# Kernel tuning notes

Hardware: AMD Instinct MI355X
Metric: run time of the kernel (lower is better)

## Reference

```python
import jax, jax.numpy as jnp
import numpy as np

B = 512      # batch (len(missing_type))
HALF = 12    # prompt_length // 3
D = 12       # prompt_depth
DT = 512     # text embed dim
DI = 768     # image embed dim
E = DT + DI  # 1280, concat dim
R = 16
H = E // R    # 80
HC = DT // R  # 32
EPS = 1e-5


def _ln(x, g, b):
    m = jnp.mean(x, -1, keepdims=True)
    v = jnp.mean((x - m) ** 2, -1, keepdims=True)
    return (x - m) * jax.lax.rsqrt(v + EPS) * g + b


def _mlp(x, w1, b1, w2, b2):
    return jax.nn.gelu(x @ w1 + b1, approximate=False) @ w2 + b2


def setup_inputs() -> dict:
    key = jax.random.key(0)
    ks = jax.random.split(key, 20)
    n = lambda k, s: jax.random.normal(k, s, dtype=jnp.float32) * 0.02
    return {
        "missing_type": jax.random.randint(ks[0], (B,), 0, 3),
        "vpc": n(ks[1], (HALF, DI)), "vpm": n(ks[2], (HALF, DI)),
        "tpc": n(ks[3], (HALF, DT)), "tpm": n(ks[4], (HALF, DT)),
        "cpc": n(ks[5], (HALF, DT)), "cpi": n(ks[6], (HALF, DT)), "cpt": n(ks[7], (HALF, DT)),
        "ln_img_g": jnp.ones((D, E)), "ln_img_b": jnp.zeros((D, E)),
        "ln_txt_g": jnp.ones((D, E)), "ln_txt_b": jnp.zeros((D, E)),
        "img_w1": n(ks[8], (D, E, H)), "img_b1": jnp.zeros((D, H)),
        "img_w2": n(ks[9], (D, H, DI)), "img_b2": jnp.zeros((D, DI)),
        "txt_w1": n(ks[10], (D, E, H)), "txt_b1": jnp.zeros((D, H)),
        "txt_w2": n(ks[11], (D, H, DT)), "txt_b2": jnp.zeros((D, DT)),
        "cimg_w1": n(ks[12], (DT, HC)), "cimg_b1": jnp.zeros((HC,)),
        "cimg_w2": n(ks[13], (HC, DI)), "cimg_b2": jnp.zeros((DI,)),
        "ctxt_w1": n(ks[14], (DT, HC)), "ctxt_b1": jnp.zeros((HC,)),
        "ctxt_w2": n(ks[15], (HC, DT)), "ctxt_b2": jnp.zeros((DT,)),
    }


def reference(missing_type, vpc, vpm, tpc, tpm, cpc, cpi, cpt,
              ln_img_g, ln_img_b, ln_txt_g, ln_txt_b,
              img_w1, img_b1, img_w2, img_b2,
              txt_w1, txt_b1, txt_w2, txt_b2,
              cimg_w1, cimg_b1, cimg_w2, cimg_b2,
              ctxt_w1, ctxt_b1, ctxt_w2, ctxt_b2):
    depth = img_w1.shape[0]
    mt = missing_type
    # per-sample branch selection, vectorized over the batch
    img = jnp.where((mt == 2)[:, None, None], vpm[None], vpc[None])  # [B,HALF,768]
    txt = jnp.where((mt == 1)[:, None, None], tpm[None], tpc[None])  # [B,HALF,512]
    common = jnp.stack([cpc, cpi, cpt])[mt]                          # [B,HALF,512]
    imgs, txts = [], []
    for d in range(depth):  # sequential depth dependency
        x = jnp.concatenate([img, txt], -1)  # [B,HALF,1280]
        img = _mlp(_ln(x, ln_img_g[d], ln_img_b[d]), img_w1[d], img_b1[d], img_w2[d], img_b2[d])
        txt = _mlp(_ln(x, ln_txt_g[d], ln_txt_b[d]), txt_w1[d], txt_b1[d], txt_w2[d], txt_b2[d])
        imgs.append(img)
        txts.append(txt)
    # depth-0 prompts get the projected common prompt appended along tokens
    img0 = jnp.concatenate([imgs[0], _mlp(common, cimg_w1, cimg_b1, cimg_w2, cimg_b2)], axis=1)
    txt0 = jnp.concatenate([txts[0], _mlp(common, ctxt_w1, ctxt_b1, ctxt_w2, ctxt_b2)], axis=1)
    return (img0, txt0, jnp.stack(imgs[1:]), jnp.stack(txts[1:]))
```

## Files before the change

### kernel.cpp

```cpp
#include <hip/hip_runtime.h>

typedef unsigned int u32;
typedef unsigned short u16;

#define TPB 640

namespace {
constexpr size_t F_WP1  = 0;
constexpr size_t F_WP2  = 1228800;
constexpr size_t F_S1   = 1843200;
constexpr size_t F_T1   = 1845120;
constexpr size_t F_XI_P = 1847040;
constexpr size_t F_XT_P = 2178816;
constexpr size_t F_CI_P = 2400000;
constexpr size_t F_CT_P = 2427648;
constexpr size_t F_END_P = 2446080;
constexpr size_t F_XI_U = 0;
constexpr size_t F_XT_U = 331776;
constexpr size_t F_CI_U = 552960;
constexpr size_t F_CT_U = 580608;
}

__device__ __forceinline__ float bflo(u32 u) { return __uint_as_float(u << 16); }
__device__ __forceinline__ float bfhi(u32 u) { return __uint_as_float(u & 0xffff0000u); }
__device__ __forceinline__ float gelu_f(float x) { return 0.5f * x * (1.0f + erff(x * 0.70710678118654752f)); }
__device__ __forceinline__ u16 f2bf(float f) {
    u32 u = __float_as_uint(f);
    u += 0x7fffu + ((u >> 16) & 1u);
    return (u16)(u >> 16);
}

struct P {
    const float *vpc, *vpm, *tpc, *tpm, *cpc, *cpi, *cpt;
    const float *lig, *lib, *ltg, *ltb;
    const float *iw1, *ib1, *iw2, *ib2;
    const float *tw1, *tb1, *tw2, *tb2;
    const float *ciw1, *cib1, *ciw2, *cib2;
    const float *ctw1, *ctb1, *ctw2, *ctb2;
    const u16 *wp1, *wp2;
    const float *s1, *t1;
    float *xi, *xt, *cimg, *ctxt;
};

__global__ __launch_bounds__(320) void prep_kernel(P p, u16* wp1o, u32* wp2o, float* s1o, float* t1o) {
    __shared__ float sA[4][80], sB[4][80];
    const int t = threadIdx.x;
    if (blockIdx.x < 24) {
        const int d = blockIdx.x >> 1, path = blockIdx.x & 1;
        const float* W1 = (path ? p.tw1 : p.iw1) + (size_t)d * 1280 * 80;
        const float* G  = (path ? p.ltg : p.lig) + d * 1280;
        const float* Bb = (path ? p.ltb : p.lib) + d * 1280;
        const int j = t % 80, kc = t / 80;
        float S = 0.f, T = 0.f;
        for (int k = kc * 320; k < kc * 320 + 320; ++k) {
            float w = W1[(size_t)k * 80 + j];
            float wg = G[k] * w;
            S += wg; T += Bb[k] * w;
            wp1o[((size_t)(d * 1280) + k) * 160 + path * 80 + j] = f2bf(wg);
        }
        sA[kc][j] = S; sB[kc][j] = T;
        __syncthreads();
        if (t < 80) {
            float Ssum = sA[0][t] + sA[1][t] + sA[2][t] + sA[3][t];
            float Tsum = sB[0][t] + sB[1][t] + sB[2][t] + sB[3][t];
            s1o[d * 160 + path * 80 + t] = Ssum;
            t1o[d * 160 + path * 80 + t] = Tsum + (path ? p.tb1 : p.ib1)[d * 80 + t];
        }
    } else {
        constexpr u32 N2 = 12u * 80 * 640;
        u32 i = (blockIdx.x - 24) * 320 + t;
        if (i >= N2) return;
        u32 c2 = i % 640, rem = i / 640;
        u32 k = rem % 80, d = rem / 80;
        u32 c0 = 2 * c2;
        const float* s = (c0 < 768) ? (p.iw2 + ((size_t)(d * 80) + k) * 768 + c0)
                                    : (p.tw2 + ((size_t)(d * 80) + k) * 512 + (c0 - 768));
        float2 v = *reinterpret_cast<const float2*>(s);
        wp2o[i] = (u32)f2bf(v.x) | ((u32)f2bf(v.y) << 16);
    }
}

__global__ __launch_bounds__(TPB) void chain2_kernel(P p) {
    __shared__ float smem[6608];
    float* sx   = smem;
    float* part = smem + 1280;
    float* hh   = smem + 6400;
    float* redA = smem + 6560;
    float* redB = smem + 6580;
    float* st   = smem + 6600;

    const int tid = threadIdx.x;
    const int blk = blockIdx.x;

    if (blk < 36) {
        const int v = blk / 12, t = blk % 12;
        const float* is = (v == 2) ? p.vpm : p.vpc;
        const float* ts = (v == 1) ? p.tpm : p.tpc;
        for (int k = tid; k < 768; k += TPB) sx[k] = is[t * 768 + k];
        if (tid < 512) sx[768 + tid] = ts[t * 512 + tid];
        __syncthreads();

        for (int d = 0; d < 12; ++d) {
            {
                float x0 = sx[tid], x1 = sx[tid + 640];
                float s = x0 + x1, s2 = x0 * x0 + x1 * x1;
                #pragma unroll
                for (int off = 32; off > 0; off >>= 1) { s += __shfl_down(s, off); s2 += __shfl_down(s2, off); }
                if ((tid & 63) == 0) { redA[tid >> 6] = s; redB[tid >> 6] = s2; }
            }
            __syncthreads();
            if (tid == 0) {
                float S = 0.f, S2 = 0.f;
                #pragma unroll
                for (int w = 0; w < 10; ++w) { S += redA[w]; S2 += redB[w]; }
                float m = S * (1.0f / 1280.0f);
                float var = S2 * (1.0f / 1280.0f) - m * m;
                st[0] = m; st[1] = rsqrtf(var + 1e-5f);
            }
            {
                const int g = tid % 20, kc = tid / 20;
                const int j0 = 8 * g, k0 = 40 * kc;
                const u16* wp = p.wp1 + ((size_t)(d * 1280) + k0) * 160 + j0;
                float a0 = 0.f, a1 = 0.f, a2 = 0.f, a3 = 0.f;
                float a4 = 0.f, a5 = 0.f, a6 = 0.f, a7 = 0.f;
                #pragma unroll 8
                for (int i = 0; i < 40; ++i) {
                    uint4 w = *reinterpret_cast<const uint4*>(wp);
                    float xv = sx[k0 + i];
                    a0 += xv * bflo(w.x); a1 += xv * bfhi(w.x);
                    a2 += xv * bflo(w.y); a3 += xv * bfhi(w.y);
                    a4 += xv * bflo(w.z); a5 += xv * bfhi(w.z);
                    a6 += xv * bflo(w.w); a7 += xv * bfhi(w.w);
                    wp += 160;
                }
                *reinterpret_cast<float4*>(part + kc * 160 + j0)     = make_float4(a0, a1, a2, a3);
                *reinterpret_cast<float4*>(part + kc * 160 + j0 + 4) = make_float4(a4, a5, a6, a7);
            }
            __syncthreads();
            if (tid < 160) {
                float y = 0.f;
                #pragma unroll
                for (int kc = 0; kc < 32; ++kc) y += part[kc * 160 + tid];
                const float m = st[0], rs = st[1];
                float hpre = rs * y - m * rs * p.s1[d * 160 + tid] + p.t1[d * 160 + tid];
                hh[tid] = gelu_f(hpre);
            }
            __syncthreads();
            {
                const int g2 = tid % 320, kc = tid / 320;
                const int c0 = 4 * g2, k0 = 40 * kc;
                const u16* wq = p.wp2 + ((size_t)(d * 80) + k0) * 1280 + c0;
                const float* hb = hh + ((c0 >= 768) ? 80 : 0);
                float a0 = 0.f, a1 = 0.f, a2 = 0.f, a3 = 0.f;
                #pragma unroll 8
                for (int i = 0; i < 40; ++i) {
                    uint2 w = *reinterpret_cast<const uint2*>(wq);
                    float hv = hb[k0 + i];
                    a0 += hv * bflo(w.x); a1 += hv * bfhi(w.x);
                    a2 += hv * bflo(w.y); a3 += hv * bfhi(w.y);
                    wq += 1280;
                }
                *reinterpret_cast<float4*>(part + kc * 1280 + c0) = make_float4(a0, a1, a2, a3);
            }
            __syncthreads();
            {
                const int c0 = 2 * tid;
                const int pth = (c0 >= 768);
                const int cc = c0 - 768 * pth;
                const int Np = pth ? 512 : 768;
                float2 bb = *reinterpret_cast<const float2*>((pth ? p.tb2 : p.ib2) + d * Np + cc);
                float a0 = part[c0]     + part[1280 + c0]     + bb.x;
                float a1 = part[c0 + 1] + part[1280 + c0 + 1] + bb.y;
                __syncthreads();
                sx[c0] = a0; sx[c0 + 1] = a1;
                float* xo = pth ? (p.xt + ((size_t)(d * 36) + blk) * 512 + cc)
                                : (p.xi + ((size_t)(d * 36) + blk) * 768 + cc);
                *reinterpret_cast<float2*>(xo) = make_float2(a0, a1);
            }
            __syncthreads();
        }
    } else {
        float* cx  = smem;
        float* ph  = smem + 512;
        float* hhl = smem + 768;
        const int rr = blk - 36, v = rr / 12, t = rr % 12;
        const float* cs = (v == 0) ? p.cpc : (v == 1) ? p.cpi : p.cpt;
        if (tid < 512) cx[tid] = cs[t * 512 + tid];
        __syncthreads();
        if (tid < 256) {
            const int o = tid & 63, kc = tid >> 6;
            const int path = o >> 5, j = o & 31;
            const float* w = (path ? p.ctw1 : p.ciw1) + (size_t)(kc * 128) * 32 + j;
            float a = 0.f;
            #pragma unroll 8
            for (int i = 0; i < 128; ++i) { a += cx[kc * 128 + i] * (*w); w += 32; }
            ph[kc * 64 + o] = a;
        }
        __syncthreads();
        if (tid < 64) {
            const int path = tid >> 5, j = tid & 31;
            float a = (path ? p.ctb1 : p.cib1)[j];
            #pragma unroll
            for (int kc = 0; kc < 4; ++kc) a += ph[kc * 64 + tid];
            hhl[tid] = gelu_f(a);
        }
        __syncthreads();
        for (int o = tid; o < 1280; o += TPB) {
            if (o < 768) {
                float a = p.cib2[o];
                #pragma unroll
                for (int k = 0; k < 32; ++k) a += hhl[k] * p.ciw2[k * 768 + o];
                p.cimg[rr * 768 + o] = a;
            } else {
                const int oo = o - 768;
                float a = p.ctb2[oo];
                #pragma unroll
                for (int k = 0; k < 32; ++k) a += hhl[32 + k] * p.ctw2[k * 512 + oo];
                p.ctxt[rr * 512 + oo] = a;
            }
        }
    }
}

__global__ __launch_bounds__(TPB) void chain_fb_kernel(P p) {
    __shared__ float smem[6592];
    float* sx   = smem;
    float* xln0 = smem + 1280;
    float* xln1 = smem + 2560;
    float* part = smem + 3840;
    float* hh   = smem + 6400;
    float* redA = smem + 6560;
    float* redB = smem + 6570;
    float* st   = smem + 6580;

    const int tid = threadIdx.x;
    const int blk = blockIdx.x;

    if (blk < 36) {
        const int v = blk / 12, t = blk % 12;
        const float* is = (v == 2) ? p.vpm : p.vpc;
        const float* ts = (v == 1) ? p.tpm : p.tpc;
        if (tid < 512) sx[768 + tid] = ts[t * 512 + tid];
        for (int k = tid; k < 768; k += TPB) sx[k] = is[t * 768 + k];
        __syncthreads();
        for (int d = 0; d < 12; ++d) {
            {
                float x0 = sx[tid], x1 = sx[tid + 640];
                float s = x0 + x1, s2 = x0 * x0 + x1 * x1;
                #pragma unroll
                for (int off = 32; off > 0; off >>= 1) { s += __shfl_down(s, off); s2 += __shfl_down(s2, off); }
                if ((tid & 63) == 0) { redA[tid >> 6] = s; redB[tid >> 6] = s2; }
            }
            __syncthreads();
            if (tid == 0) {
                float S = 0.f, S2 = 0.f;
                #pragma unroll
                for (int w = 0; w < 10; ++w) { S += redA[w]; S2 += redB[w]; }
                float m = S * (1.0f / 1280.0f);
                float var = S2 * (1.0f / 1280.0f) - m * m;
                st[0] = m; st[1] = rsqrtf(var + 1e-5f);
            }
            __syncthreads();
            const float m = st[0], rs = st[1];
            #pragma unroll
            for (int q = 0; q < 2; ++q) {
                const int k = tid + 640 * q;
                float xc = (sx[k] - m) * rs;
                xln0[k] = xc * p.lig[d * 1280 + k] + p.lib[d * 1280 + k];
                xln1[k] = xc * p.ltg[d * 1280 + k] + p.ltb[d * 1280 + k];
            }
            __syncthreads();
            {
                const int g = tid % 40, kc = tid / 40;
                const int j0 = 4 * g;
                const float* xl = (j0 >= 80) ? xln1 : xln0;
                const int k0 = kc * 80;
                float a0 = 0.f, a1 = 0.f, a2 = 0.f, a3 = 0.f;
                const float* wp = (j0 < 80) ? (p.iw1 + ((size_t)(d * 1280) + k0) * 80 + j0)
                                            : (p.tw1 + ((size_t)(d * 1280) + k0) * 80 + (j0 - 80));
                #pragma unroll 8
                for (int i = 0; i < 80; ++i) {
                    float4 w = *reinterpret_cast<const float4*>(wp);
                    float xv = xl[k0 + i];
                    a0 += xv * w.x; a1 += xv * w.y; a2 += xv * w.z; a3 += xv * w.w;
                    wp += 80;
                }
                *reinterpret_cast<float4*>(part + kc * 160 + j0) = make_float4(a0, a1, a2, a3);
            }
            __syncthreads();
            if (tid < 160) {
                const int path = tid >= 80, j = tid - 80 * path;
                float a = (path ? p.tb1 : p.ib1)[d * 80 + j];
                #pragma unroll
                for (int kc = 0; kc < 16; ++kc) a += part[kc * 160 + tid];
                hh[tid] = gelu_f(a);
            }
            __syncthreads();
            {
                const int c = tid;
                const int pth = (c >= 384);
                const int cc = 2 * c - 768 * pth;
                const float* hb = hh + 80 * pth;
                const int Np = pth ? 512 : 768;
                const float* b2 = (pth ? p.tb2 : p.ib2) + d * Np + cc;
                float a0 = b2[0], a1 = b2[1];
                const float* wp = (pth ? p.tw2 + (size_t)(d * 80) * 512 : p.iw2 + (size_t)(d * 80) * 768) + cc;
                #pragma unroll 16
                for (int k = 0; k < 80; ++k) {
                    float2 w = *reinterpret_cast<const float2*>(wp);
                    float hv = hb[k];
                    a0 += hv * w.x; a1 += hv * w.y;
                    wp += Np;
                }
                sx[2 * c] = a0; sx[2 * c + 1] = a1;
                float* xo = pth ? (p.xt + ((size_t)(d * 36) + blk) * 512 + cc)
                                : (p.xi + ((size_t)(d * 36) + blk) * 768 + cc);
                *reinterpret_cast<float2*>(xo) = make_float2(a0, a1);
            }
            __syncthreads();
        }
    } else {
        float* cx  = smem;
        float* ph  = smem + 512;
        float* hhl = smem + 768;
        const int rr = blk - 36, v = rr / 12, t = rr % 12;
        const float* cs = (v == 0) ? p.cpc : (v == 1) ? p.cpi : p.cpt;
        if (tid < 512) cx[tid] = cs[t * 512 + tid];
        __syncthreads();
        if (tid < 256) {
            const int o = tid & 63, kc = tid >> 6;
            const int path = o >> 5, j = o & 31;
            const float* w = (path ? p.ctw1 : p.ciw1) + (size_t)(kc * 128) * 32 + j;
            float a = 0.f;
            #pragma unroll 8
            for (int i = 0; i < 128; ++i) { a += cx[kc * 128 + i] * (*w); w += 32; }
            ph[kc * 64 + o] = a;
        }
        __syncthreads();
        if (tid < 64) {
            const int path = tid >> 5, j = tid & 31;
            float a = (path ? p.ctb1 : p.cib1)[j];
            #pragma unroll
            for (int kc = 0; kc < 4; ++kc) a += ph[kc * 64 + tid];
            hhl[tid] = gelu_f(a);
        }
        __syncthreads();
        for (int o = tid; o < 1280; o += TPB) {
            if (o < 768) {
                float a = p.cib2[o];
                #pragma unroll
                for (int k = 0; k < 32; ++k) a += hhl[k] * p.ciw2[k * 768 + o];
                p.cimg[rr * 768 + o] = a;
            } else {
                const int oo = o - 768;
                float a = p.ctb2[oo];
                #pragma unroll
                for (int k = 0; k < 32; ++k) a += hhl[32 + k] * p.ctw2[k * 512 + oo];
                p.ctxt[rr * 512 + oo] = a;
            }
        }
    }
}

__global__ __launch_bounds__(256) void emit_kernel(const int* __restrict__ mt,
                                                   const float* __restrict__ xi,
                                                   const float* __restrict__ xt,
                                                   const float* __restrict__ cimg,
                                                   const float* __restrict__ ctxt,
                                                   float* __restrict__ out) {
    constexpr unsigned int C0 = 512u * 24 * 192;
    constexpr unsigned int C1 = 512u * 24 * 128;
    constexpr unsigned int C2 = 11u * 512 * 12 * 192;
    constexpr unsigned int C3 = 11u * 512 * 12 * 128;
    constexpr unsigned int TOT = C0 + C1 + C2 + C3;
    const unsigned int stride = gridDim.x * blockDim.x;
    for (unsigned int c = blockIdx.x * blockDim.x + threadIdx.x; c < TOT; c += stride) {
        const float* src;
        if (c < C0) {
            unsigned int b = c / 4608u, r = c % 4608u;
            unsigned int tok = r / 192u, col = (r % 192u) * 4u;
            int v = mt[b];
            src = (tok < 12u) ? xi + ((size_t)v * 12 + tok) * 768 + col
                              : cimg + ((size_t)v * 12 + (tok - 12u)) * 768 + col;
        } else if (c < C0 + C1) {
            unsigned int cc = c - C0;
            unsigned int b = cc / 3072u, r = cc % 3072u;
            unsigned int tok = r / 128u, col = (r % 128u) * 4u;
            int v = mt[b];
            src = (tok < 12u) ? xt + ((size_t)v * 12 + tok) * 512 + col
                              : ctxt + ((size_t)v * 12 + (tok - 12u)) * 512 + col;
        } else if (c < C0 + C1 + C2) {
            unsigned int cc = c - C0 - C1;
            unsigned int d = cc / 1179648u, r = cc % 1179648u;
            unsigned int b = r / 2304u, rr = r % 2304u;
            unsigned int tok = rr / 192u, col = (rr % 192u) * 4u;
            int v = mt[b];
            src = xi + ((size_t)(d + 1) * 36 + v * 12 + tok) * 768 + col;
        } else {
            unsigned int cc = c - C0 - C1 - C2;
            unsigned int d = cc / 786432u, r = cc % 786432u;
            unsigned int b = r / 1536u, rr = r % 1536u;
            unsigned int tok = rr / 128u, col = (rr % 128u) * 4u;
            int v = mt[b];
            src = xt + ((size_t)(d + 1) * 36 + v * 12 + tok) * 512 + col;
        }
        *reinterpret_cast<float4*>(out + (size_t)c * 4) = *reinterpret_cast<const float4*>(src);
    }
}

extern "C" void kernel_launch(void* const* d_in, const int* in_sizes, int n_in,
                              void* d_out, int out_size, void* d_ws, size_t ws_size,
                              hipStream_t stream) {
    const int* mt = (const int*)d_in[0];
    float* ws = (float*)d_ws;
    P p;
    p.vpc  = (const float*)d_in[1];
    p.vpm  = (const float*)d_in[2];
    p.tpc  = (const float*)d_in[3];
    p.tpm  = (const float*)d_in[4];
    p.cpc  = (const float*)d_in[5];
    p.cpi  = (const float*)d_in[6];
    p.cpt  = (const float*)d_in[7];
    p.lig  = (const float*)d_in[8];
    p.lib  = (const float*)d_in[9];
    p.ltg  = (const float*)d_in[10];
    p.ltb  = (const float*)d_in[11];
    p.iw1  = (const float*)d_in[12];
    p.ib1  = (const float*)d_in[13];
    p.iw2  = (const float*)d_in[14];
    p.ib2  = (const float*)d_in[15];
    p.tw1  = (const float*)d_in[16];
    p.tb1  = (const float*)d_in[17];
    p.tw2  = (const float*)d_in[18];
    p.tb2  = (const float*)d_in[19];
    p.ciw1 = (const float*)d_in[20];
    p.cib1 = (const float*)d_in[21];
    p.ciw2 = (const float*)d_in[22];
    p.cib2 = (const float*)d_in[23];
    p.ctw1 = (const float*)d_in[24];
    p.ctb1 = (const float*)d_in[25];
    p.ctw2 = (const float*)d_in[26];
    p.ctb2 = (const float*)d_in[27];

    const bool packed = (ws_size >= F_END_P * sizeof(float));
    if (packed) {
        p.wp1  = (const u16*)(ws + F_WP1);
        p.wp2  = (const u16*)(ws + F_WP2);
        p.s1   = ws + F_S1;
        p.t1   = ws + F_T1;
        p.xi   = ws + F_XI_P;
        p.xt   = ws + F_XT_P;
        p.cimg = ws + F_CI_P;
        p.ctxt = ws + F_CT_P;
        constexpr u32 N2 = 12u * 80 * 640;
        const int nb = 24 + (N2 + 319) / 320;
        prep_kernel<<<dim3(nb), dim3(320), 0, stream>>>(p, (u16*)(ws + F_WP1), (u32*)(ws + F_WP2),
                                                        ws + F_S1, ws + F_T1);
        chain2_kernel<<<dim3(72), dim3(TPB), 0, stream>>>(p);
    } else {
        p.wp1 = nullptr; p.wp2 = nullptr; p.s1 = nullptr; p.t1 = nullptr;
        p.xi   = ws + F_XI_U;
        p.xt   = ws + F_XT_U;
        p.cimg = ws + F_CI_U;
        p.ctxt = ws + F_CT_U;
        chain_fb_kernel<<<dim3(72), dim3(TPB), 0, stream>>>(p);
    }
    emit_kernel<<<dim3(4096), dim3(256), 0, stream>>>(mt, p.xi, p.xt, p.cimg, p.ctxt, (float*)d_out);
}
```

Before: 268.4 us.

## Stream per-depth bf16 weight slots into LDS with double-buffered async loads

Repacks both MLP weight matrices into one contiguous per-depth blob of fifteen 40KB slots. The chain kernel prefetches the next slot into LDS with global_load_lds while computing on the current one, replacing direct strided global weight reads. The prep work is split into a fully parallel pack kernel and a separate LN-fold reduction kernel, and the second GEMV no longer needs a cross-thread partial sum. This adds a barrier and vmcnt wait per slot, about 92KB of dynamic LDS per block, and an extra kernel launch.

```diff
diff --git a/kernel.cpp b/kernel.cpp
--- a/kernel.cpp
+++ b/kernel.cpp
@@ -4,21 +4,20 @@
 typedef unsigned short u16;
 
 #define TPB 640
+#define NSLOT_TOT 180
+#define SLOT_F32 10240
+#define CHAIN_DYN 92928
 
 namespace {
-constexpr size_t F_WP1  = 0;
-constexpr size_t F_WP2  = 1228800;
+constexpr size_t F_BLOB = 0;
 constexpr size_t F_S1   = 1843200;
 constexpr size_t F_T1   = 1845120;
-constexpr size_t F_XI_P = 1847040;
-constexpr size_t F_XT_P = 2178816;
-constexpr size_t F_CI_P = 2400000;
-constexpr size_t F_CT_P = 2427648;
-constexpr size_t F_END_P = 2446080;
-constexpr size_t F_XI_U = 0;
-constexpr size_t F_XT_U = 331776;
-constexpr size_t F_CI_U = 552960;
-constexpr size_t F_CT_U = 580608;
+constexpr size_t F_XI   = 1847040;
+constexpr size_t F_XT   = 2178816;
+constexpr size_t F_CI   = 2400000;
+constexpr size_t F_CT   = 2427648;
+constexpr size_t F_END  = 2446080;
+constexpr size_t F_XI_U = 0, F_XT_U = 331776, F_CI_U = 552960, F_CT_U = 580608;
 }
 
 __device__ __forceinline__ float bflo(u32 u) { return __uint_as_float(u << 16); }
@@ -37,68 +36,104 @@
     const float *tw1, *tb1, *tw2, *tb2;
     const float *ciw1, *cib1, *ciw2, *cib2;
     const float *ctw1, *ctb1, *ctw2, *ctb2;
-    const u16 *wp1, *wp2;
+    const u16 *blob;
     const float *s1, *t1;
     float *xi, *xt, *cimg, *ctxt;
 };
 
-__global__ __launch_bounds__(320) void prep_kernel(P p, u16* wp1o, u32* wp2o, float* s1o, float* t1o) {
-    __shared__ float sA[4][80], sB[4][80];
-    const int t = threadIdx.x;
-    if (blockIdx.x < 24) {
-        const int d = blockIdx.x >> 1, path = blockIdx.x & 1;
-        const float* W1 = (path ? p.tw1 : p.iw1) + (size_t)d * 1280 * 80;
-        const float* G  = (path ? p.ltg : p.lig) + d * 1280;
-        const float* Bb = (path ? p.ltb : p.lib) + d * 1280;
-        const int j = t % 80, kc = t / 80;
-        float S = 0.f, T = 0.f;
-        for (int k = kc * 320; k < kc * 320 + 320; ++k) {
-            float w = W1[(size_t)k * 80 + j];
-            float wg = G[k] * w;
-            S += wg; T += Bb[k] * w;
-            wp1o[((size_t)(d * 1280) + k) * 160 + path * 80 + j] = f2bf(wg);
-        }
-        sA[kc][j] = S; sB[kc][j] = T;
-        __syncthreads();
-        if (t < 80) {
-            float Ssum = sA[0][t] + sA[1][t] + sA[2][t] + sA[3][t];
-            float Tsum = sB[0][t] + sB[1][t] + sB[2][t] + sB[3][t];
-            s1o[d * 160 + path * 80 + t] = Ssum;
-            t1o[d * 160 + path * 80 + t] = Tsum + (path ? p.tb1 : p.ib1)[d * 80 + t];
-        }
+__global__ __launch_bounds__(256) void prep_pack_kernel(P p, u32* blob32) {
+    constexpr u32 N1 = 12u * 1280 * 80;
+    constexpr u32 N2 = 12u * 80 * 640;
+    u32 i = blockIdx.x * 256 + threadIdx.x;
+    if (i < N1) {
+        u32 j2 = i % 80, rem = i / 80;
+        u32 k = rem % 1280, d = rem / 1280;
+        u32 j0 = 2 * j2;
+        const int path = (j0 >= 80);
+        const float* W = (path ? p.tw1 : p.iw1) + ((size_t)(d * 1280) + k) * 80 + (j0 - 80 * path);
+        float g = (path ? p.ltg : p.lig)[d * 1280 + k];
+        float2 v = *reinterpret_cast<const float2*>(W);
+        blob32[(size_t)d * 153600 + (size_t)k * 80 + j2] =
+            (u32)f2bf(g * v.x) | ((u32)f2bf(g * v.y) << 16);
     } else {
-        constexpr u32 N2 = 12u * 80 * 640;
-        u32 i = (blockIdx.x - 24) * 320 + t;
-        if (i >= N2) return;
-        u32 c2 = i % 640, rem = i / 640;
+        u32 ii = i - N1;
+        if (ii >= N2) return;
+        u32 c2 = ii % 640, rem = ii / 640;
         u32 k = rem % 80, d = rem / 80;
         u32 c0 = 2 * c2;
         const float* s = (c0 < 768) ? (p.iw2 + ((size_t)(d * 80) + k) * 768 + c0)
                                     : (p.tw2 + ((size_t)(d * 80) + k) * 512 + (c0 - 768));
         float2 v = *reinterpret_cast<const float2*>(s);
-        wp2o[i] = (u32)f2bf(v.x) | ((u32)f2bf(v.y) << 16);
-    }
-}
-
-__global__ __launch_bounds__(TPB) void chain2_kernel(P p) {
-    __shared__ float smem[6608];
-    float* sx   = smem;
-    float* part = smem + 1280;
-    float* hh   = smem + 6400;
-    float* redA = smem + 6560;
-    float* redB = smem + 6580;
-    float* st   = smem + 6600;
-
+        blob32[(size_t)d * 153600 + 102400 + (size_t)k * 640 + c2] =
+            (u32)f2bf(v.x) | ((u32)f2bf(v.y) << 16);
+    }
+}
+
+__global__ __launch_bounds__(TPB) void prep_fold_kernel(P p, float* s1o, float* t1o) {
+    __shared__ float sA[8][80], sB[8][80];
     const int tid = threadIdx.x;
-    const int blk = blockIdx.x;
+    const int d = blockIdx.x >> 1, path = blockIdx.x & 1;
+    const float* W1 = (path ? p.tw1 : p.iw1) + (size_t)d * 1280 * 80;
+    const float* G  = (path ? p.ltg : p.lig) + d * 1280;
+    const float* Bb = (path ? p.ltb : p.lib) + d * 1280;
+    const int j = tid % 80, kc = tid / 80;
+    float S = 0.f, T = 0.f;
+    for (int k = kc * 160; k < kc * 160 + 160; ++k) {
+        float w = W1[(size_t)k * 80 + j];
+        S += G[k] * w; T += Bb[k] * w;
+    }
+    sA[kc][j] = S; sB[kc][j] = T;
+    __syncthreads();
+    if (tid < 80) {
+        float Ss = 0.f, Ts = 0.f;
+        #pragma unroll
+        for (int q = 0; q < 8; ++q) { Ss += sA[q][tid]; Ts += sB[q][tid]; }
+        s1o[d * 160 + path * 80 + tid] = Ss;
+        t1o[d * 160 + path * 80 + tid] = Ts + (path ? p.tb1 : p.ib1)[d * 80 + tid];
+    }
+}
+
+__device__ __forceinline__ void stage_slot(const u16* blob, float* buf, int sigma) {
+    const int d = sigma / 15, s = sigma % 15;
+    const char* gbase = (const char*)(blob + (size_t)d * 307200
+                                      + (s < 10 ? (size_t)s * 20480 : 204800 + (size_t)(s - 10) * 20480));
+    char* lbase = (char*)buf;
+    const int lane = threadIdx.x & 63, wave = threadIdx.x >> 6;
+    #pragma unroll
+    for (int r = 0; r < 4; ++r) {
+        const int q = r * 10 + wave;
+        __builtin_amdgcn_global_load_lds(
+            (const __attribute__((address_space(1))) void*)(gbase + q * 1024 + lane * 16),
+            (__attribute__((address_space(3))) void*)(lbase + q * 1024), 16, 0, 0);
+    }
+}
+
+#define SLOT_SYNC do { asm volatile("s_waitcnt vmcnt(0)" ::: "memory"); \
+                       __builtin_amdgcn_sched_barrier(0); __syncthreads(); } while (0)
+
+__global__ __launch_bounds__(TPB) void chain4_kernel(P p) {
+    extern __shared__ float smem[];
+    float* buf0 = smem;
+    float* buf1 = smem + 10240;
+    float* sx   = smem + 20480;
+    float* part = smem + 21760;
+    float* hh   = smem + 23040;
+    float* redA = smem + 23200;
+    float* redB = smem + 23210;
+    float* st   = smem + 23220;
+
+    const int tid = threadIdx.x, blk = blockIdx.x;
 
     if (blk < 36) {
         const int v = blk / 12, t = blk % 12;
+        stage_slot(p.blob, buf0, 0);
         const float* is = (v == 2) ? p.vpm : p.vpc;
         const float* ts = (v == 1) ? p.tpm : p.tpc;
         for (int k = tid; k < 768; k += TPB) sx[k] = is[t * 768 + k];
         if (tid < 512) sx[768 + tid] = ts[t * 512 + tid];
-        __syncthreads();
+        SLOT_SYNC;
+        int cur = 0;
+        const int jp = tid % 80, kc = tid / 80;
 
         for (int d = 0; d < 12; ++d) {
             {
@@ -117,65 +152,53 @@
                 float var = S2 * (1.0f / 1280.0f) - m * m;
                 st[0] = m; st[1] = rsqrtf(var + 1e-5f);
             }
-            {
-                const int g = tid % 20, kc = tid / 20;
-                const int j0 = 8 * g, k0 = 40 * kc;
-                const u16* wp = p.wp1 + ((size_t)(d * 1280) + k0) * 160 + j0;
-                float a0 = 0.f, a1 = 0.f, a2 = 0.f, a3 = 0.f;
-                float a4 = 0.f, a5 = 0.f, a6 = 0.f, a7 = 0.f;
-                #pragma unroll 8
-                for (int i = 0; i < 40; ++i) {
-                    uint4 w = *reinterpret_cast<const uint4*>(wp);
-                    float xv = sx[k0 + i];
-                    a0 += xv * bflo(w.x); a1 += xv * bfhi(w.x);
-                    a2 += xv * bflo(w.y); a3 += xv * bfhi(w.y);
-                    a4 += xv * bflo(w.z); a5 += xv * bfhi(w.z);
-                    a6 += xv * bflo(w.w); a7 += xv * bfhi(w.w);
-                    wp += 160;
+            float a0 = 0.f, a1 = 0.f, b0 = 0.f, b1 = 0.f;
+            for (int s = 0; s < 10; ++s) {
+                const int sig = d * 15 + s;
+                if (sig + 1 < NSLOT_TOT) stage_slot(p.blob, cur ? buf0 : buf1, sig + 1);
+                const u32* wp = (const u32*)(cur ? buf1 : buf0) + kc * 1280 + jp;
+                const float* xs = sx + s * 128 + kc * 16;
+                #pragma unroll
+                for (int i = 0; i < 16; ++i) {
+                    u32 w = wp[i * 80];
+                    float xv = xs[i];
+                    a0 += xv * bflo(w); a1 += xv * bfhi(w);
                 }
-                *reinterpret_cast<float4*>(part + kc * 160 + j0)     = make_float4(a0, a1, a2, a3);
-                *reinterpret_cast<float4*>(part + kc * 160 + j0 + 4) = make_float4(a4, a5, a6, a7);
-            }
-            __syncthreads();
+                if (s == 9) { part[kc * 160 + 2 * jp] = a0; part[kc * 160 + 2 * jp + 1] = a1; }
+                SLOT_SYNC; cur ^= 1;
+            }
             if (tid < 160) {
                 float y = 0.f;
                 #pragma unroll
-                for (int kc = 0; kc < 32; ++kc) y += part[kc * 160 + tid];
+                for (int q = 0; q < 8; ++q) y += part[q * 160 + tid];
                 const float m = st[0], rs = st[1];
-                float hpre = rs * y - m * rs * p.s1[d * 160 + tid] + p.t1[d * 160 + tid];
-                hh[tid] = gelu_f(hpre);
-            }
-            __syncthreads();
-            {
-                const int g2 = tid % 320, kc = tid / 320;
-                const int c0 = 4 * g2, k0 = 40 * kc;
-                const u16* wq = p.wp2 + ((size_t)(d * 80) + k0) * 1280 + c0;
-                const float* hb = hh + ((c0 >= 768) ? 80 : 0);
-                float a0 = 0.f, a1 = 0.f, a2 = 0.f, a3 = 0.f;
-                #pragma unroll 8
-                for (int i = 0; i < 40; ++i) {
-                    uint2 w = *reinterpret_cast<const uint2*>(wq);
-                    float hv = hb[k0 + i];
-                    a0 += hv * bflo(w.x); a1 += hv * bfhi(w.x);
-                    a2 += hv * bflo(w.y); a3 += hv * bfhi(w.y);
-                    wq += 1280;
+                hh[tid] = gelu_f(rs * y - m * rs * p.s1[d * 160 + tid] + p.t1[d * 160 + tid]);
+            }
+            __syncthreads();
+            for (int s = 10; s < 15; ++s) {
+                const int sig = d * 15 + s;
+                if (sig + 1 < NSLOT_TOT) stage_slot(p.blob, cur ? buf0 : buf1, sig + 1);
+                const u32* wq = (const u32*)(cur ? buf1 : buf0) + tid;
+                const float* hb = hh + ((tid >= 384) ? 80 : 0) + (s - 10) * 16;
+                #pragma unroll
+                for (int i = 0; i < 16; ++i) {
+                    u32 w = wq[i * 640];
+                    float hv = hb[i];
+                    b0 += hv * bflo(w); b1 += hv * bfhi(w);
                 }
-                *reinterpret_cast<float4*>(part + kc * 1280 + c0) = make_float4(a0, a1, a2, a3);
-            }
-            __syncthreads();
+                SLOT_SYNC; cur ^= 1;
+            }
             {
                 const int c0 = 2 * tid;
                 const int pth = (c0 >= 768);
                 const int cc = c0 - 768 * pth;
                 const int Np = pth ? 512 : 768;
-                float2 bb = *reinterpret_cast<const float2*>((pth ? p.tb2 : p.ib2) + d * Np + cc);
-                float a0 = part[c0]     + part[1280 + c0]     + bb.x;
-                float a1 = part[c0 + 1] + part[1280 + c0 + 1] + bb.y;
-                __syncthreads();
-                sx[c0] = a0; sx[c0 + 1] = a1;
+                const float* bb = (pth ? p.tb2 : p.ib2) + d * Np + cc;
+                float o0 = b0 + bb[0], o1 = b1 + bb[1];
+                sx[c0] = o0; sx[c0 + 1] = o1;
                 float* xo = pth ? (p.xt + ((size_t)(d * 36) + blk) * 512 + cc)
                                 : (p.xi + ((size_t)(d * 36) + blk) * 768 + cc);
-                *reinterpret_cast<float2*>(xo) = make_float2(a0, a1);
+                *reinterpret_cast<float2*>(xo) = make_float2(o0, o1);
             }
             __syncthreads();
         }
@@ -188,20 +211,20 @@
         if (tid < 512) cx[tid] = cs[t * 512 + tid];
         __syncthreads();
         if (tid < 256) {
-            const int o = tid & 63, kc = tid >> 6;
+            const int o = tid & 63, kcq = tid >> 6;
             const int path = o >> 5, j = o & 31;
-            const float* w = (path ? p.ctw1 : p.ciw1) + (size_t)(kc * 128) * 32 + j;
+            const float* w = (path ? p.ctw1 : p.ciw1) + (size_t)(kcq * 128) * 32 + j;
             float a = 0.f;
             #pragma unroll 8
-            for (int i = 0; i < 128; ++i) { a += cx[kc * 128 + i] * (*w); w += 32; }
-            ph[kc * 64 + o] = a;
+            for (int i = 0; i < 128; ++i) { a += cx[kcq * 128 + i] * (*w); w += 32; }
+            ph[kcq * 64 + o] = a;
         }
         __syncthreads();
         if (tid < 64) {
             const int path = tid >> 5, j = tid & 31;
             float a = (path ? p.ctb1 : p.cib1)[j];
             #pragma unroll
-            for (int kc = 0; kc < 4; ++kc) a += ph[kc * 64 + tid];
+            for (int q = 0; q < 4; ++q) a += ph[q * 64 + tid];
             hhl[tid] = gelu_f(a);
         }
         __syncthreads();
@@ -232,10 +255,7 @@
     float* redA = smem + 6560;
     float* redB = smem + 6570;
     float* st   = smem + 6580;
-
-    const int tid = threadIdx.x;
-    const int blk = blockIdx.x;
-
+    const int tid = threadIdx.x, blk = blockIdx.x;
     if (blk < 36) {
         const int v = blk / 12, t = blk % 12;
         const float* is = (v == 2) ? p.vpm : p.vpc;
@@ -271,10 +291,10 @@
             }
             __syncthreads();
             {
-                const int g = tid % 40, kc = tid / 40;
+                const int g = tid % 40, kcq = tid / 40;
                 const int j0 = 4 * g;
                 const float* xl = (j0 >= 80) ? xln1 : xln0;
-                const int k0 = kc * 80;
+                const int k0 = kcq * 80;
                 float a0 = 0.f, a1 = 0.f, a2 = 0.f, a3 = 0.f;
                 const float* wp = (j0 < 80) ? (p.iw1 + ((size_t)(d * 1280) + k0) * 80 + j0)
                                             : (p.tw1 + ((size_t)(d * 1280) + k0) * 80 + (j0 - 80));
@@ -285,14 +305,14 @@
                     a0 += xv * w.x; a1 += xv * w.y; a2 += xv * w.z; a3 += xv * w.w;
                     wp += 80;
                 }
-                *reinterpret_cast<float4*>(part + kc * 160 + j0) = make_float4(a0, a1, a2, a3);
+                *reinterpret_cast<float4*>(part + kcq * 160 + j0) = make_float4(a0, a1, a2, a3);
             }
             __syncthreads();
             if (tid < 160) {
                 const int path = tid >= 80, j = tid - 80 * path;
                 float a = (path ? p.tb1 : p.ib1)[d * 80 + j];
                 #pragma unroll
-                for (int kc = 0; kc < 16; ++kc) a += part[kc * 160 + tid];
+                for (int q = 0; q < 16; ++q) a += part[q * 160 + tid];
                 hh[tid] = gelu_f(a);
             }
             __syncthreads();
@@ -328,20 +348,20 @@
         if (tid < 512) cx[tid] = cs[t * 512 + tid];
         __syncthreads();
         if (tid < 256) {
-            const int o = tid & 63, kc = tid >> 6;
+            const int o = tid & 63, kcq = tid >> 6;
             const int path = o >> 5, j = o & 31;
-            const float* w = (path ? p.ctw1 : p.ciw1) + (size_t)(kc * 128) * 32 + j;
+            const float* w = (path ? p.ctw1 : p.ciw1) + (size_t)(kcq * 128) * 32 + j;
             float a = 0.f;
             #pragma unroll 8
-            for (int i = 0; i < 128; ++i) { a += cx[kc * 128 + i] * (*w); w += 32; }
-            ph[kc * 64 + o] = a;
+            for (int i = 0; i < 128; ++i) { a += cx[kcq * 128 + i] * (*w); w += 32; }
+            ph[kcq * 64 + o] = a;
         }
         __syncthreads();
         if (tid < 64) {
             const int path = tid >> 5, j = tid & 31;
             float a = (path ? p.ctb1 : p.cib1)[j];
             #pragma unroll
-            for (int kc = 0; kc < 4; ++kc) a += ph[kc * 64 + tid];
+            for (int q = 0; q < 4; ++q) a += ph[q * 64 + tid];
             hhl[tid] = gelu_f(a);
         }
         __syncthreads();
@@ -442,23 +462,23 @@
     p.ctw2 = (const float*)d_in[26];
     p.ctb2 = (const float*)d_in[27];
 
-    const bool packed = (ws_size >= F_END_P * sizeof(float));
+    const bool packed = (ws_size >= F_END * sizeof(float));
     if (packed) {
-        p.wp1  = (const u16*)(ws + F_WP1);
-        p.wp2  = (const u16*)(ws + F_WP2);
+        p.blob = (const u16*)(ws + F_BLOB);
         p.s1   = ws + F_S1;
         p.t1   = ws + F_T1;
-        p.xi   = ws + F_XI_P;
-        p.xt   = ws + F_XT_P;
-        p.cimg = ws + F_CI_P;
-        p.ctxt = ws + F_CT_P;
-        constexpr u32 N2 = 12u * 80 * 640;
-        const int nb = 24 + (N2 + 319) / 320;
-        prep_kernel<<<dim3(nb), dim3(320), 0, stream>>>(p, (u16*)(ws + F_WP1), (u32*)(ws + F_WP2),
-                                                        ws + F_S1, ws + F_T1);
-        chain2_kernel<<<dim3(72), dim3(TPB), 0, stream>>>(p);
+        p.xi   = ws + F_XI;
+        p.xt   = ws + F_XT;
+        p.cimg = ws + F_CI;
+        p.ctxt = ws + F_CT;
+        constexpr u32 NPAIR = 12u * 1280 * 80 + 12u * 80 * 640;
+        prep_pack_kernel<<<dim3((NPAIR + 255) / 256), dim3(256), 0, stream>>>(p, (u32*)(ws + F_BLOB));
+        prep_fold_kernel<<<dim3(24), dim3(TPB), 0, stream>>>(p, ws + F_S1, ws + F_T1);
+        hipFuncSetAttribute((const void*)chain4_kernel,
+                            hipFuncAttributeMaxDynamicSharedMemorySize, CHAIN_DYN);
+        chain4_kernel<<<dim3(72), dim3(TPB), CHAIN_DYN, stream>>>(p);
     } else {
-        p.wp1 = nullptr; p.wp2 = nullptr; p.s1 = nullptr; p.t1 = nullptr;
+        p.blob = nullptr; p.s1 = nullptr; p.t1 = nullptr;
         p.xi   = ws + F_XI_U;
         p.xt   = ws + F_XT_U;
         p.cimg = ws + F_CI_U;
```

Measured after the change: 252.4 us. 1.06x faster.
